# Kernel tuning notes

Measured on AMD Instinct MI355X. Metric: run time of the kernel, lower is better.

## Reference

```python
import jax, jax.numpy as jnp
import numpy as np

N = 50000        # nodes
E = 600000       # edges
F_IN = 128       # num_node_features
H = 128          # hidden_channels
G = 2000         # number of graphs (batch segments)
C = 1            # num_classes
EPS = 1e-5       # BatchNorm eps


def setup_inputs() -> dict:
    key = jax.random.key(0)
    ks = jax.random.split(key, 12)
    x = jax.random.normal(ks[0], (N, F_IN), dtype=jnp.float32)
    edge_index = jax.random.randint(ks[1], (2, E), 0, N, dtype=jnp.int32)
    batch = jnp.sort(jax.random.randint(ks[2], (N,), 0, G, dtype=jnp.int32))
    s = 0.05
    W1 = jax.random.normal(ks[3], (F_IN, H), dtype=jnp.float32) * s
    b1 = jnp.zeros((H,), dtype=jnp.float32)
    W2 = jax.random.normal(ks[4], (H, H), dtype=jnp.float32) * s
    b2 = jnp.zeros((H,), dtype=jnp.float32)
    W3 = jax.random.normal(ks[5], (H, H), dtype=jnp.float32) * s
    b3 = jnp.zeros((H,), dtype=jnp.float32)
    # BatchNorm (eval mode): running stats + affine params, stacked [3, H]
    bn_gamma = jnp.ones((3, H), dtype=jnp.float32)
    bn_beta = jnp.zeros((3, H), dtype=jnp.float32)
    bn_mean = jnp.zeros((3, H), dtype=jnp.float32)
    bn_var = jnp.ones((3, H), dtype=jnp.float32)
    lin1_W = jax.random.normal(ks[6], (3 * H, H), dtype=jnp.float32) * s
    lin1_b = jnp.zeros((H,), dtype=jnp.float32)
    lin2_W = jax.random.normal(ks[7], (H, C), dtype=jnp.float32) * s
    lin2_b = jnp.zeros((C,), dtype=jnp.float32)
    return {"x": x, "edge_index": edge_index, "batch": batch,
            "W1": W1, "b1": b1, "W2": W2, "b2": b2, "W3": W3, "b3": b3,
            "bn_gamma": bn_gamma, "bn_beta": bn_beta, "bn_mean": bn_mean, "bn_var": bn_var,
            "lin1_W": lin1_W, "lin1_b": lin1_b, "lin2_W": lin2_W, "lin2_b": lin2_b}


def _gcn_norm(edge_index):
    # Add self loops, compute symmetric normalization D^-1/2 (A+I) D^-1/2.
    loop = jnp.arange(N, dtype=edge_index.dtype)
    row = jnp.concatenate([edge_index[0], loop])   # sources (E+N,)
    col = jnp.concatenate([edge_index[1], loop])   # targets (E+N,)
    deg = jax.ops.segment_sum(jnp.ones(E + N, dtype=jnp.float32), col, num_segments=N)
    dinv = jnp.where(deg > 0, jax.lax.rsqrt(deg), 0.0)
    norm = dinv[row] * dinv[col]                   # (E+N,)
    return row, col, norm


def _gcn_conv(h, W, b, row, col, norm):
    h = h @ W                                      # [N, H] transform first (PyG GCNConv)
    msg = h[row] * norm[:, None]                   # edge-wise gather + scale
    out = jax.ops.segment_sum(msg, col, num_segments=N)  # scatter-add aggregate
    return out + b


def _bn_relu(h, g, b, m, v):
    return jax.nn.relu((h - m) * jax.lax.rsqrt(v + EPS) * g + b)


def reference(x, edge_index, batch, W1, b1, W2, b2, W3, b3,
              bn_gamma, bn_beta, bn_mean, bn_var,
              lin1_W, lin1_b, lin2_W, lin2_b):
    row, col, norm = _gcn_norm(edge_index)
    h = _bn_relu(_gcn_conv(x, W1, b1, row, col, norm), bn_gamma[0], bn_beta[0], bn_mean[0], bn_var[0])
    h = _bn_relu(_gcn_conv(h, W2, b2, row, col, norm), bn_gamma[1], bn_beta[1], bn_mean[1], bn_var[1])
    h = _bn_relu(_gcn_conv(h, W3, b3, row, col, norm), bn_gamma[2], bn_beta[2], bn_mean[2], bn_var[2])
    # Multi-pool over ragged graph segments
    seg = batch
    x_sum = jax.ops.segment_sum(h, seg, num_segments=G)                 # [G, H]
    cnt = jax.ops.segment_sum(jnp.ones((N,), dtype=h.dtype), seg, num_segments=G)
    x_mean = x_sum / jnp.maximum(cnt, 1.0)[:, None]
    x_max = jax.ops.segment_max(h, seg, num_segments=G)
    x_max = jnp.where(jnp.isfinite(x_max), x_max, 0.0)                  # empty segments -> 0
    z = jnp.concatenate([x_mean, x_max, x_sum], axis=1)                 # [G, 3H]
    z = jax.nn.relu(z @ lin1_W + lin1_b)
    return z @ lin2_W + lin2_b                                          # [G, C]
```

## Files before the change

kernel.cpp:

```cpp
#include <hip/hip_runtime.h>
#include <cfloat>
#include <cstdint>

#define N_NODES 50000
#define N_EDGES 600000
#define HDIM    128
#define NGRAPH  2000
#define BN_EPS  1e-5f


__global__ void k_init(int* degi, int* seg_s, int* seg_e) {
    int i = blockIdx.x * 256 + threadIdx.x;
    if (i < N_NODES) degi[i] = 1;
    if (i < NGRAPH) { seg_s[i] = 0x7FFFFFFF; seg_e[i] = 0; }
}

__global__ void k_count(const int* __restrict__ ei, int* degi) {
    int e = blockIdx.x * 256 + threadIdx.x;
    if (e < N_EDGES) atomicAdd(&degi[ei[N_EDGES + e]], 1);
}

__global__ void k_dinv(const int* __restrict__ degi, float* dinv) {
    int i = blockIdx.x * 256 + threadIdx.x;
    if (i < N_NODES) dinv[i] = rsqrtf((float)degi[i]);
}

__global__ void k_scanA(const int* __restrict__ degi, int* ptr, int* bsum) {
    __shared__ int t[256];
    int i = blockIdx.x * 256 + threadIdx.x;
    int v = (i < N_NODES) ? degi[i] : 0;
    t[threadIdx.x] = v; __syncthreads();
    for (int off = 1; off < 256; off <<= 1) {
        int a = (threadIdx.x >= off) ? t[threadIdx.x - off] : 0;
        __syncthreads();
        t[threadIdx.x] += a;
        __syncthreads();
    }
    if (i < N_NODES) ptr[i + 1] = t[threadIdx.x];
    if (threadIdx.x == 255) bsum[blockIdx.x] = t[255];
}

__global__ void k_scanB(const int* __restrict__ bsum, int* boff, int nb) {
    __shared__ int t[256];
    int i = threadIdx.x;
    int v = (i < nb) ? bsum[i] : 0;
    t[i] = v; __syncthreads();
    for (int off = 1; off < 256; off <<= 1) {
        int a = (i >= off) ? t[i - off] : 0;
        __syncthreads();
        t[i] += a;
        __syncthreads();
    }
    if (i < nb) boff[i] = t[i] - v;
}

__global__ void k_scanC(int* ptr, const int* __restrict__ boff, int* cursor) {
    int i = blockIdx.x * 256 + threadIdx.x;
    if (i < N_NODES) {
        int val = ptr[i + 1] + boff[blockIdx.x];
        ptr[i + 1] = val;
        if (i + 1 < N_NODES) cursor[i + 1] = val;
    }
    if (i == 0) { ptr[0] = 0; cursor[0] = 0; }
}

__global__ void k_fill(const int* __restrict__ ei, const float* __restrict__ dinv,
                       int* cursor, int2* meta) {
    int e = blockIdx.x * 256 + threadIdx.x;
    if (e < N_EDGES) {
        int r = ei[e], c = ei[N_EDGES + e];
        int pos = atomicAdd(&cursor[c], 1);
        meta[pos] = make_int2(r, __float_as_int(dinv[r] * dinv[c]));
    } else if (e < N_EDGES + N_NODES) {
        int v = e - N_EDGES;
        int pos = atomicAdd(&cursor[v], 1);
        float d = dinv[v];
        meta[pos] = make_int2(v, __float_as_int(d * d));
    }
}

__global__ void k_seg(const int* __restrict__ batch, int* seg_s, int* seg_e) {
    int i = blockIdx.x * 256 + threadIdx.x;
    if (i < N_NODES) {
        int g = batch[i];
        atomicMin(&seg_s[g], i);
        atomicMax(&seg_e[g], i + 1);
    }
}


__global__ __launch_bounds__(256) void k_transform(const float4* __restrict__ hin4,
                                                   const float4* __restrict__ W4,
                                                   float4* __restrict__ hout4) {
    __shared__ float4 Hs[32 * 32];
    size_t g4 = (size_t)blockIdx.x * 1024;
#pragma unroll
    for (int p = 0; p < 4; p++) {
        int idx = threadIdx.x + p * 256;
        if (g4 + idx < (size_t)N_NODES * 32) Hs[idx] = hin4[g4 + idx];
    }
    __syncthreads();

    int ct = threadIdx.x & 31;
    int nt = threadIdx.x >> 5;
    int base = blockIdx.x * 32;

    float4 acc0 = make_float4(0.f, 0.f, 0.f, 0.f);
    float4 acc1 = acc0, acc2 = acc0, acc3 = acc0;

#pragma unroll 4
    for (int kc = 0; kc < 32; kc++) {
        float4 ha = Hs[(nt * 4 + 0) * 32 + kc];
        float4 hb = Hs[(nt * 4 + 1) * 32 + kc];
        float4 hc = Hs[(nt * 4 + 2) * 32 + kc];
        float4 hd = Hs[(nt * 4 + 3) * 32 + kc];
        float4 w0 = W4[(kc * 4 + 0) * 32 + ct];
        float4 w1 = W4[(kc * 4 + 1) * 32 + ct];
        float4 w2 = W4[(kc * 4 + 2) * 32 + ct];
        float4 w3 = W4[(kc * 4 + 3) * 32 + ct];

        acc0.x += ha.x * w0.x + ha.y * w1.x + ha.z * w2.x + ha.w * w3.x;
        acc0.y += ha.x * w0.y + ha.y * w1.y + ha.z * w2.y + ha.w * w3.y;
        acc0.z += ha.x * w0.z + ha.y * w1.z + ha.z * w2.z + ha.w * w3.z;
        acc0.w += ha.x * w0.w + ha.y * w1.w + ha.z * w2.w + ha.w * w3.w;

        acc1.x += hb.x * w0.x + hb.y * w1.x + hb.z * w2.x + hb.w * w3.x;
        acc1.y += hb.x * w0.y + hb.y * w1.y + hb.z * w2.y + hb.w * w3.y;
        acc1.z += hb.x * w0.z + hb.y * w1.z + hb.z * w2.z + hb.w * w3.z;
        acc1.w += hb.x * w0.w + hb.y * w1.w + hb.z * w2.w + hb.w * w3.w;

        acc2.x += hc.x * w0.x + hc.y * w1.x + hc.z * w2.x + hc.w * w3.x;
        acc2.y += hc.x * w0.y + hc.y * w1.y + hc.z * w2.y + hc.w * w3.y;
        acc2.z += hc.x * w0.z + hc.y * w1.z + hc.z * w2.z + hc.w * w3.z;
        acc2.w += hc.x * w0.w + hc.y * w1.w + hc.z * w2.w + hc.w * w3.w;

        acc3.x += hd.x * w0.x + hd.y * w1.x + hd.z * w2.x + hd.w * w3.x;
        acc3.y += hd.x * w0.y + hd.y * w1.y + hd.z * w2.y + hd.w * w3.y;
        acc3.z += hd.x * w0.z + hd.y * w1.z + hd.z * w2.z + hd.w * w3.z;
        acc3.w += hd.x * w0.w + hd.y * w1.w + hd.z * w2.w + hd.w * w3.w;
    }

    int n0 = base + nt * 4;
    if (n0 + 0 < N_NODES) hout4[(size_t)(n0 + 0) * 32 + ct] = acc0;
    if (n0 + 1 < N_NODES) hout4[(size_t)(n0 + 1) * 32 + ct] = acc1;
    if (n0 + 2 < N_NODES) hout4[(size_t)(n0 + 2) * 32 + ct] = acc2;
    if (n0 + 3 < N_NODES) hout4[(size_t)(n0 + 3) * 32 + ct] = acc3;
}


__global__ __launch_bounds__(256) void k_aggregate(const float4* __restrict__ h4,
                                                   const int* __restrict__ ptr,
                                                   const int2* __restrict__ meta,
                                                   const float4* __restrict__ bias4,
                                                   const float4* __restrict__ bng4,
                                                   const float4* __restrict__ bnb4,
                                                   const float4* __restrict__ bnm4,
                                                   const float4* __restrict__ bnv4,
                                                   float4* __restrict__ hout4) {
    int v = blockIdx.x * 8 + (threadIdx.x >> 5);
    int c = threadIdx.x & 31;
    if (v >= N_NODES) return;
    int e0 = ptr[v], e1 = ptr[v + 1];

    float ax = 0.f, ay = 0.f, az = 0.f, aw = 0.f;
    int j = e0;
    for (; j + 4 <= e1; j += 4) {
        int2 m0 = meta[j], m1 = meta[j + 1], m2 = meta[j + 2], m3 = meta[j + 3];
        float4 v0 = h4[(size_t)m0.x * 32 + c];
        float4 v1 = h4[(size_t)m1.x * 32 + c];
        float4 v2 = h4[(size_t)m2.x * 32 + c];
        float4 v3 = h4[(size_t)m3.x * 32 + c];
        float n0 = __int_as_float(m0.y), n1 = __int_as_float(m1.y);
        float n2 = __int_as_float(m2.y), n3 = __int_as_float(m3.y);
        ax += n0 * v0.x + n1 * v1.x + n2 * v2.x + n3 * v3.x;
        ay += n0 * v0.y + n1 * v1.y + n2 * v2.y + n3 * v3.y;
        az += n0 * v0.z + n1 * v1.z + n2 * v2.z + n3 * v3.z;
        aw += n0 * v0.w + n1 * v1.w + n2 * v2.w + n3 * v3.w;
    }
    int rem = e1 - j;
    if (rem > 0) {
        int i1 = j + (rem > 1 ? 1 : 0);
        int i2 = j + (rem > 2 ? 2 : 0);
        int2 m0 = meta[j], m1 = meta[i1], m2 = meta[i2];
        float4 v0 = h4[(size_t)m0.x * 32 + c];
        float4 v1 = h4[(size_t)m1.x * 32 + c];
        float4 v2 = h4[(size_t)m2.x * 32 + c];
        float n0 = __int_as_float(m0.y);
        float n1 = (rem > 1) ? __int_as_float(m1.y) : 0.f;
        float n2 = (rem > 2) ? __int_as_float(m2.y) : 0.f;
        ax += n0 * v0.x + n1 * v1.x + n2 * v2.x;
        ay += n0 * v0.y + n1 * v1.y + n2 * v2.y;
        az += n0 * v0.z + n1 * v1.z + n2 * v2.z;
        aw += n0 * v0.w + n1 * v1.w + n2 * v2.w;
    }

    float4 bs = bias4[c], g = bng4[c], bb = bnb4[c], m = bnm4[c], vv = bnv4[c];
    float sx = g.x * rsqrtf(vv.x + BN_EPS), tx = bb.x - m.x * sx;
    float sy = g.y * rsqrtf(vv.y + BN_EPS), ty = bb.y - m.y * sy;
    float sz = g.z * rsqrtf(vv.z + BN_EPS), tz = bb.z - m.z * sz;
    float sw = g.w * rsqrtf(vv.w + BN_EPS), tw = bb.w - m.w * sw;
    float4 r;
    r.x = fmaxf((ax + bs.x) * sx + tx, 0.f);
    r.y = fmaxf((ay + bs.y) * sy + ty, 0.f);
    r.z = fmaxf((az + bs.z) * sz + tz, 0.f);
    r.w = fmaxf((aw + bs.w) * sw + tw, 0.f);
    hout4[(size_t)v * 32 + c] = r;
}


__global__ __launch_bounds__(128) void k_pool(const float* __restrict__ h,
                                              const int* __restrict__ seg_s,
                                              const int* __restrict__ seg_e,
                                              const float* __restrict__ l1W,
                                              const float* __restrict__ l1b,
                                              const float* __restrict__ l2W,
                                              const float* __restrict__ l2b,
                                              float* __restrict__ out) {
    __shared__ float z[3 * HDIM];
    __shared__ float red[2];
    int g = blockIdx.x, c = threadIdx.x;
    int s = seg_s[g], e = seg_e[g];
    float sum = 0.f, mx = -FLT_MAX;
    for (int i = s; i < e; i++) {
        float val = h[(size_t)i * HDIM + c];
        sum += val;
        mx = fmaxf(mx, val);
    }
    int cnt = (s < e) ? (e - s) : 0;
    if (cnt == 0) { mx = 0.f; sum = 0.f; }
    float mean = sum / (float)(cnt > 1 ? cnt : 1);
    z[c] = mean; z[HDIM + c] = mx; z[2 * HDIM + c] = sum;
    __syncthreads();
    float o = l1b[c];
    for (int k = 0; k < 3 * HDIM; k++) o += z[k] * l1W[k * HDIM + c];
    o = fmaxf(o, 0.f);
    float p = o * l2W[c];
#pragma unroll
    for (int off = 32; off; off >>= 1) p += __shfl_down(p, off, 64);
    if ((c & 63) == 0) red[c >> 6] = p;
    __syncthreads();
    if (c == 0) out[g] = red[0] + red[1] + l2b[0];
}


extern "C" void kernel_launch(void* const* d_in, const int* in_sizes, int n_in,
                              void* d_out, int out_size, void* d_ws, size_t ws_size,
                              hipStream_t stream) {
    const float* x   = (const float*)d_in[0];
    const int*   ei  = (const int*)d_in[1];
    const int*   bat = (const int*)d_in[2];
    const float* W1  = (const float*)d_in[3];
    const float* b1  = (const float*)d_in[4];
    const float* W2  = (const float*)d_in[5];
    const float* b2  = (const float*)d_in[6];
    const float* W3  = (const float*)d_in[7];
    const float* b3  = (const float*)d_in[8];
    const float* bng = (const float*)d_in[9];
    const float* bnb = (const float*)d_in[10];
    const float* bnm = (const float*)d_in[11];
    const float* bnv = (const float*)d_in[12];
    const float* l1W = (const float*)d_in[13];
    const float* l1b = (const float*)d_in[14];
    const float* l2W = (const float*)d_in[15];
    const float* l2b = (const float*)d_in[16];
    float* out = (float*)d_out;

    char* ws = (char*)d_ws;
    size_t off = 0;
    auto alloc = [&](size_t bytes) -> char* {
        char* p = ws + off;
        off = (off + bytes + 255) & ~(size_t)255;
        return p;
    };
    int*   degi   = (int*)alloc((size_t)N_NODES * 4);
    float* dinv   = (float*)alloc((size_t)N_NODES * 4);
    int*   ptr    = (int*)alloc((size_t)(N_NODES + 1) * 4);
    int*   cursor = (int*)alloc((size_t)N_NODES * 4);
    int*   bsum   = (int*)alloc(256 * 4);
    int*   boff   = (int*)alloc(256 * 4);
    int*   seg_s  = (int*)alloc((size_t)NGRAPH * 4);
    int*   seg_e  = (int*)alloc((size_t)NGRAPH * 4);
    int2*  meta   = (int2*)alloc((size_t)(N_EDGES + N_NODES) * 8);
    float* hA     = (float*)alloc((size_t)N_NODES * HDIM * 4);
    float* hB     = (float*)alloc((size_t)N_NODES * HDIM * 4);
    (void)ws_size;

    int nblk = (N_NODES + 255) / 256;

    k_init<<<nblk, 256, 0, stream>>>(degi, seg_s, seg_e);
    k_count<<<(N_EDGES + 255) / 256, 256, 0, stream>>>(ei, degi);
    k_dinv<<<nblk, 256, 0, stream>>>(degi, dinv);
    k_scanA<<<nblk, 256, 0, stream>>>(degi, ptr, bsum);
    k_scanB<<<1, 256, 0, stream>>>(bsum, boff, nblk);
    k_scanC<<<nblk, 256, 0, stream>>>(ptr, boff, cursor);
    k_fill<<<(N_EDGES + N_NODES + 255) / 256, 256, 0, stream>>>(ei, dinv, cursor, meta);
    k_seg<<<nblk, 256, 0, stream>>>(bat, seg_s, seg_e);

    int tb = (N_NODES + 31) / 32;
    int ab = (N_NODES + 7) / 8;

    k_transform<<<tb, 256, 0, stream>>>((const float4*)x, (const float4*)W1, (float4*)hA);
    k_aggregate<<<ab, 256, 0, stream>>>((const float4*)hA, ptr, meta, (const float4*)b1,
                                        (const float4*)(bng + 0), (const float4*)(bnb + 0),
                                        (const float4*)(bnm + 0), (const float4*)(bnv + 0),
                                        (float4*)hB);
    k_transform<<<tb, 256, 0, stream>>>((const float4*)hB, (const float4*)W2, (float4*)hA);
    k_aggregate<<<ab, 256, 0, stream>>>((const float4*)hA, ptr, meta, (const float4*)b2,
                                        (const float4*)(bng + HDIM), (const float4*)(bnb + HDIM),
                                        (const float4*)(bnm + HDIM), (const float4*)(bnv + HDIM),
                                        (float4*)hB);
    k_transform<<<tb, 256, 0, stream>>>((const float4*)hB, (const float4*)W3, (float4*)hA);
    k_aggregate<<<ab, 256, 0, stream>>>((const float4*)hA, ptr, meta, (const float4*)b3,
                                        (const float4*)(bng + 2 * HDIM), (const float4*)(bnb + 2 * HDIM),
                                        (const float4*)(bnm + 2 * HDIM), (const float4*)(bnv + 2 * HDIM),
                                        (float4*)hB);

    k_pool<<<NGRAPH, 128, 0, stream>>>(hB, seg_s, seg_e, l1W, l1b, l2W, l2b, out);
}
```

Measured before the change: 350.8 us.

## Fuse preprocessing kernels, widen aggregate gather batch to 8, vectorize pool matvec

New measurement: 346.9 us. No clear change (-1.1%).

```diff
diff --git a/kernel.cpp b/kernel.cpp
--- a/kernel.cpp
+++ b/kernel.cpp
@@ -15,20 +15,22 @@
     if (i < NGRAPH) { seg_s[i] = 0x7FFFFFFF; seg_e[i] = 0; }
 }
 
-__global__ void k_count(const int* __restrict__ ei, int* degi) {
+__global__ void k_count_seg(const int* __restrict__ ei, int* degi,
+                            const int* __restrict__ batch, int* seg_s, int* seg_e) {
     int e = blockIdx.x * 256 + threadIdx.x;
     if (e < N_EDGES) atomicAdd(&degi[ei[N_EDGES + e]], 1);
-}
-
-__global__ void k_dinv(const int* __restrict__ degi, float* dinv) {
-    int i = blockIdx.x * 256 + threadIdx.x;
-    if (i < N_NODES) dinv[i] = rsqrtf((float)degi[i]);
-}
-
-__global__ void k_scanA(const int* __restrict__ degi, int* ptr, int* bsum) {
+    if (e < N_NODES) {
+        int g = batch[e];
+        atomicMin(&seg_s[g], e);
+        atomicMax(&seg_e[g], e + 1);
+    }
+}
+
+__global__ void k_scanA(const int* __restrict__ degi, int* ptr, int* bsum, float* dinv) {
     __shared__ int t[256];
     int i = blockIdx.x * 256 + threadIdx.x;
     int v = (i < N_NODES) ? degi[i] : 0;
+    if (i < N_NODES) dinv[i] = rsqrtf((float)v);
     t[threadIdx.x] = v; __syncthreads();
     for (int off = 1; off < 256; off <<= 1) {
         int a = (threadIdx.x >= off) ? t[threadIdx.x - off] : 0;
@@ -76,15 +78,6 @@
         int pos = atomicAdd(&cursor[v], 1);
         float d = dinv[v];
         meta[pos] = make_int2(v, __float_as_int(d * d));
-    }
-}
-
-__global__ void k_seg(const int* __restrict__ batch, int* seg_s, int* seg_e) {
-    int i = blockIdx.x * 256 + threadIdx.x;
-    if (i < N_NODES) {
-        int g = batch[i];
-        atomicMin(&seg_s[g], i);
-        atomicMax(&seg_e[g], i + 1);
     }
 }
 
@@ -164,34 +157,34 @@
 
     float ax = 0.f, ay = 0.f, az = 0.f, aw = 0.f;
     int j = e0;
-    for (; j + 4 <= e1; j += 4) {
-        int2 m0 = meta[j], m1 = meta[j + 1], m2 = meta[j + 2], m3 = meta[j + 3];
-        float4 v0 = h4[(size_t)m0.x * 32 + c];
-        float4 v1 = h4[(size_t)m1.x * 32 + c];
-        float4 v2 = h4[(size_t)m2.x * 32 + c];
-        float4 v3 = h4[(size_t)m3.x * 32 + c];
-        float n0 = __int_as_float(m0.y), n1 = __int_as_float(m1.y);
-        float n2 = __int_as_float(m2.y), n3 = __int_as_float(m3.y);
-        ax += n0 * v0.x + n1 * v1.x + n2 * v2.x + n3 * v3.x;
-        ay += n0 * v0.y + n1 * v1.y + n2 * v2.y + n3 * v3.y;
-        az += n0 * v0.z + n1 * v1.z + n2 * v2.z + n3 * v3.z;
-        aw += n0 * v0.w + n1 * v1.w + n2 * v2.w + n3 * v3.w;
+    for (; j + 8 <= e1; j += 8) {
+        int2 m[8];
+#pragma unroll
+        for (int i = 0; i < 8; i++) m[i] = meta[j + i];
+        float4 vv[8];
+#pragma unroll
+        for (int i = 0; i < 8; i++) vv[i] = h4[(size_t)m[i].x * 32 + c];
+#pragma unroll
+        for (int i = 0; i < 8; i++) {
+            float n = __int_as_float(m[i].y);
+            ax += n * vv[i].x; ay += n * vv[i].y;
+            az += n * vv[i].z; aw += n * vv[i].w;
+        }
     }
     int rem = e1 - j;
-    if (rem > 0) {
-        int i1 = j + (rem > 1 ? 1 : 0);
-        int i2 = j + (rem > 2 ? 2 : 0);
-        int2 m0 = meta[j], m1 = meta[i1], m2 = meta[i2];
-        float4 v0 = h4[(size_t)m0.x * 32 + c];
-        float4 v1 = h4[(size_t)m1.x * 32 + c];
-        float4 v2 = h4[(size_t)m2.x * 32 + c];
-        float n0 = __int_as_float(m0.y);
-        float n1 = (rem > 1) ? __int_as_float(m1.y) : 0.f;
-        float n2 = (rem > 2) ? __int_as_float(m2.y) : 0.f;
-        ax += n0 * v0.x + n1 * v1.x + n2 * v2.x;
-        ay += n0 * v0.y + n1 * v1.y + n2 * v2.y;
-        az += n0 * v0.z + n1 * v1.z + n2 * v2.z;
-        aw += n0 * v0.w + n1 * v1.w + n2 * v2.w;
+    if (rem) {
+        int2 m[8];
+#pragma unroll
+        for (int i = 0; i < 8; i++) m[i] = meta[j + (i < rem ? i : 0)];
+        float4 vv[8];
+#pragma unroll
+        for (int i = 0; i < 8; i++) vv[i] = h4[(size_t)m[i].x * 32 + c];
+#pragma unroll
+        for (int i = 0; i < 8; i++) {
+            float n = (i < rem) ? __int_as_float(m[i].y) : 0.f;
+            ax += n * vv[i].x; ay += n * vv[i].y;
+            az += n * vv[i].z; aw += n * vv[i].w;
+        }
     }
 
     float4 bs = bias4[c], g = bng4[c], bb = bnb4[c], m = bnm4[c], vv = bnv4[c];
@@ -231,8 +224,17 @@
     float mean = sum / (float)(cnt > 1 ? cnt : 1);
     z[c] = mean; z[HDIM + c] = mx; z[2 * HDIM + c] = sum;
     __syncthreads();
+    const float4* z4 = (const float4*)z;
     float o = l1b[c];
-    for (int k = 0; k < 3 * HDIM; k++) o += z[k] * l1W[k * HDIM + c];
+#pragma unroll 4
+    for (int k4 = 0; k4 < 96; k4++) {
+        float4 zz = z4[k4];
+        float w0 = l1W[(k4 * 4 + 0) * HDIM + c];
+        float w1 = l1W[(k4 * 4 + 1) * HDIM + c];
+        float w2 = l1W[(k4 * 4 + 2) * HDIM + c];
+        float w3 = l1W[(k4 * 4 + 3) * HDIM + c];
+        o += zz.x * w0 + zz.y * w1 + zz.z * w2 + zz.w * w3;
+    }
     o = fmaxf(o, 0.f);
     float p = o * l2W[c];
 #pragma unroll
@@ -288,13 +290,11 @@
     int nblk = (N_NODES + 255) / 256;
 
     k_init<<<nblk, 256, 0, stream>>>(degi, seg_s, seg_e);
-    k_count<<<(N_EDGES + 255) / 256, 256, 0, stream>>>(ei, degi);
-    k_dinv<<<nblk, 256, 0, stream>>>(degi, dinv);
-    k_scanA<<<nblk, 256, 0, stream>>>(degi, ptr, bsum);
+    k_count_seg<<<(N_EDGES + 255) / 256, 256, 0, stream>>>(ei, degi, bat, seg_s, seg_e);
+    k_scanA<<<nblk, 256, 0, stream>>>(degi, ptr, bsum, dinv);
     k_scanB<<<1, 256, 0, stream>>>(bsum, boff, nblk);
     k_scanC<<<nblk, 256, 0, stream>>>(ptr, boff, cursor);
     k_fill<<<(N_EDGES + N_NODES + 255) / 256, 256, 0, stream>>>(ei, dinv, cursor, meta);
-    k_seg<<<nblk, 256, 0, stream>>>(bat, seg_s, seg_e);
 
     int tb = (N_NODES + 31) / 32;
     int ab = (N_NODES + 7) / 8;
```
